# Kernel optimization log

Hardware: AMD Instinct MI355X
Metric: run time of the kernel (lower is better)

## Reference

```python
import jax, jax.numpy as jnp
from jax import lax
import numpy as np

EMBED = 1024
HIDDEN = 1024
VOCAB = 32000
T = 64


def setup_inputs() -> dict:
    key = jax.random.key(0)
    ks = jax.random.split(key, 8)
    s = 0.02  # weight init scale
    return {
        "captions": jax.random.randint(ks[0], (T,), 0, VOCAB, dtype=jnp.int32),
        "features": jax.random.normal(ks[1], (EMBED,), dtype=jnp.float32),
        "embed_table": jax.random.normal(ks[2], (VOCAB, EMBED), dtype=jnp.float32) * s,
        "W_ih": jax.random.normal(ks[3], (4 * HIDDEN, EMBED), dtype=jnp.float32) * s,
        "W_hh": jax.random.normal(ks[4], (4 * HIDDEN, HIDDEN), dtype=jnp.float32) * s,
        "b_ih": jnp.zeros((4 * HIDDEN,), dtype=jnp.float32),
        "b_hh": jnp.zeros((4 * HIDDEN,), dtype=jnp.float32),
        "fc_W": jax.random.normal(ks[5], (VOCAB, HIDDEN), dtype=jnp.float32) * s,
        "fc_b": jnp.zeros((VOCAB,), dtype=jnp.float32),
    }


def reference(captions, features, embed_table, W_ih, W_hh, b_ih, b_hh, fc_W, fc_b):
    # Embedding lookup for all caption tokens: [T, E]
    emb = embed_table[captions]
    # Input at t=0 is the visual feature; at t>0 it is embed(captions[t-1]).
    xs = jnp.concatenate([features[None, :], emb[:-1]], axis=0)  # [T, E]
    H = W_hh.shape[1]
    bias = b_ih + b_hh  # fuse the two LSTMCell biases

    def step(carry, x):
        h, c = carry  # [H], [H]  (batch = 1, kept 1-D)
        gates = x @ W_ih.T + h @ W_hh.T + bias  # [4H]
        i, f, g, o = jnp.split(gates, 4)  # PyTorch gate order: i, f, g, o
        i = jax.nn.sigmoid(i)
        f = jax.nn.sigmoid(f)
        g = jnp.tanh(g)
        o = jax.nn.sigmoid(o)
        c = f * c + i * g
        h = o * jnp.tanh(c)
        return (h, c), h

    h0 = jnp.zeros((H,), dtype=features.dtype)
    (_, _), hs = lax.scan(step, (h0, h0), xs)  # hs: [T, H]
    # Per-step Linear, expressed as one batched GEMM over all timesteps.
    logits = hs @ fc_W.T + fc_b  # [T, V]
    return logits[None, :, :]  # [1, T, V] to match outputs[:, t, :]
```

## Files before the change

kernel.cpp:

```cpp
#include <hip/hip_runtime.h>
#include <math.h>

#define EMBED  1024
#define HIDDEN 1024
#define VOCAB  32000
#define TSTEPS 64
#define NBLK   256

__global__ __launch_bounds__(256, 1) void decoder_fused(
    const int*   __restrict__ caps,
    const float* __restrict__ feat,
    const float* __restrict__ table,
    const float* __restrict__ Wih,
    const float* __restrict__ Whh,
    const float* __restrict__ bih,
    const float* __restrict__ bhh,
    const float* __restrict__ fcW,
    const float* __restrict__ fcb,
    unsigned long long* hs_pk,
    float* __restrict__ out)
{
    __shared__ __align__(16) char arena[52224];
    __shared__ float xg_s[TSTEPS][16];
    __shared__ float h_s[2][HIDDEN];
    __shared__ int   caps_s[TSTEPS];

    int tid = threadIdx.x;
    int b   = blockIdx.x;

    int lane = tid & 63;
    int wv   = tid >> 6;
    int g    = lane >> 4;
    int c16  = lane & 15;
    int hj   = 4 * b + wv;
    const float4* wrow = (const float4*)(Whh + ((size_t)g * HIDDEN + hj) * HIDDEN);
    float4 wreg[16];
#pragma unroll
    for (int k = 0; k < 16; ++k) wreg[k] = wrow[c16 + 16 * k];

    if (tid < TSTEPS) caps_s[tid] = caps[tid];

    float (*xs_s)[132] = (float (*)[132])arena;
    float (*w16)[132]  = (float (*)[132])(arena + 33792);
    int jl = tid & 15;
    int tg = tid >> 4;
    float acc4[4] = {0.f, 0.f, 0.f, 0.f};
    __syncthreads();

    for (int c = 0; c < 8; ++c) {
        __syncthreads();
        for (int idx = tid; idx < 64 * 32; idx += 256) {
            int r = idx >> 5, f4 = idx & 31;
            const float* src = (r == 0)
                ? (feat + c * 128)
                : (table + (size_t)caps_s[r - 1] * EMBED + c * 128);
            *((float4*)&xs_s[r][f4 * 4]) = ((const float4*)src)[f4];
        }
        for (int idx = tid; idx < 16 * 32; idx += 256) {
            int r = idx >> 5, f4 = idx & 31;
            int jr = (r >> 2) * HIDDEN + 4 * b + (r & 3);
            *((float4*)&w16[r][f4 * 4]) =
                ((const float4*)(Wih + (size_t)jr * EMBED + c * 128))[f4];
        }
        __syncthreads();
        for (int f4 = 0; f4 < 32; ++f4) {
            float4 w = *((const float4*)&w16[jl][f4 * 4]);
#pragma unroll
            for (int k = 0; k < 4; ++k) {
                const float* xr = &xs_s[tg * 4 + k][f4 * 4];
                acc4[k] += w.x * xr[0] + w.y * xr[1] + w.z * xr[2] + w.w * xr[3];
            }
        }
    }
    {
        int jrow = (jl >> 2) * HIDDEN + 4 * b + (jl & 3);
        float bias = bih[jrow] + bhh[jrow];
#pragma unroll
        for (int k = 0; k < 4; ++k) xg_s[tg * 4 + k][jl] = acc4[k] + bias;
    }
    __syncthreads();

    float cstate = 0.f;
    for (int t = 0; t < TSTEPS; ++t) {
        float* dst = h_s[t & 1];
        if (t == 0) {
            for (int i = tid; i < HIDDEN; i += 256) dst[i] = 0.f;
        } else {
            const unsigned long long* hsrc = hs_pk + (size_t)(t - 1) * HIDDEN;
            unsigned want = (unsigned)t;
            unsigned long long x0 = 0, x1 = 0, x2 = 0, x3 = 0;
            int need = 0xF;
            do {
                if (need & 1) {
                    x0 = __hip_atomic_load(hsrc + tid, __ATOMIC_RELAXED,
                                           __HIP_MEMORY_SCOPE_AGENT);
                    if ((unsigned)(x0 >> 32) == want) need &= ~1;
                }
                if (need & 2) {
                    x1 = __hip_atomic_load(hsrc + tid + 256, __ATOMIC_RELAXED,
                                           __HIP_MEMORY_SCOPE_AGENT);
                    if ((unsigned)(x1 >> 32) == want) need &= ~2;
                }
                if (need & 4) {
                    x2 = __hip_atomic_load(hsrc + tid + 512, __ATOMIC_RELAXED,
                                           __HIP_MEMORY_SCOPE_AGENT);
                    if ((unsigned)(x2 >> 32) == want) need &= ~4;
                }
                if (need & 8) {
                    x3 = __hip_atomic_load(hsrc + tid + 768, __ATOMIC_RELAXED,
                                           __HIP_MEMORY_SCOPE_AGENT);
                    if ((unsigned)(x3 >> 32) == want) need &= ~8;
                }
                if (need) __builtin_amdgcn_s_sleep(1);
            } while (need);
            dst[tid]       = __uint_as_float((unsigned)x0);
            dst[tid + 256] = __uint_as_float((unsigned)x1);
            dst[tid + 512] = __uint_as_float((unsigned)x2);
            dst[tid + 768] = __uint_as_float((unsigned)x3);
        }
        __syncthreads();

        float4 a = {0.f, 0.f, 0.f, 0.f};
#pragma unroll
        for (int k = 0; k < 16; ++k) {
            float4 w = wreg[k];
            const float* hv = &dst[(c16 + 16 * k) * 4];
            a.x += w.x * hv[0];
            a.y += w.y * hv[1];
            a.z += w.z * hv[2];
            a.w += w.w * hv[3];
        }
        float sum = (a.x + a.y) + (a.z + a.w);
        sum += __shfl_xor(sum, 1);
        sum += __shfl_xor(sum, 2);
        sum += __shfl_xor(sum, 4);
        sum += __shfl_xor(sum, 8);
        float s0 = __shfl(sum, 0);
        float s1 = __shfl(sum, 16);
        float s2 = __shfl(sum, 32);
        float s3 = __shfl(sum, 48);

        if (lane == 0) {
            float gi = s0 + xg_s[t][wv];
            float gf = s1 + xg_s[t][4 + wv];
            float gg = s2 + xg_s[t][8 + wv];
            float go = s3 + xg_s[t][12 + wv];
            float i_ = 1.f / (1.f + expf(-gi));
            float f_ = 1.f / (1.f + expf(-gf));
            float g_ = tanhf(gg);
            float o_ = 1.f / (1.f + expf(-go));
            cstate = f_ * cstate + i_ * g_;
            float hv = o_ * tanhf(cstate);
            unsigned long long pk =
                ((unsigned long long)(unsigned)(t + 1) << 32) |
                (unsigned long long)__float_as_uint(hv);
            __hip_atomic_store(hs_pk + (size_t)t * HIDDEN + hj, pk,
                               __ATOMIC_RELAXED, __HIP_MEMORY_SCOPE_AGENT);
        }
    }
    __syncthreads();

    if (b >= 250) return;
    float (*hs_s)[68]  = (float (*)[68])arena;
    float (*w_s3)[68]  = (float (*)[68])(arena + 17408);
    int tv = tid & 15;
    int tq = tid >> 4;
    int v0 = b * 128;
    float acc[4][8];
#pragma unroll
    for (int i = 0; i < 4; ++i)
#pragma unroll
        for (int j = 0; j < 8; ++j) acc[i][j] = 0.f;

    for (int kc = 0; kc < 16; ++kc) {
        __syncthreads();
        for (int idx = tid; idx < 64 * 64; idx += 256) {
            int t = idx >> 6, j = idx & 63;
            unsigned want = (unsigned)(t + 1);
            unsigned long long x;
            for (;;) {
                x = __hip_atomic_load(hs_pk + (size_t)t * HIDDEN + kc * 64 + j,
                                      __ATOMIC_RELAXED, __HIP_MEMORY_SCOPE_AGENT);
                if ((unsigned)(x >> 32) == want) break;
                __builtin_amdgcn_s_sleep(1);
            }
            hs_s[t][j] = __uint_as_float((unsigned)x);
        }
        for (int idx = tid; idx < 128 * 16; idx += 256) {
            int r = idx >> 4, f4 = idx & 15;
            *((float4*)&w_s3[r][f4 * 4]) =
                ((const float4*)(fcW + (size_t)(v0 + r) * HIDDEN + kc * 64))[f4];
        }
        __syncthreads();
        for (int q = 0; q < 16; ++q) {
            float4 hv4[4];
#pragma unroll
            for (int i = 0; i < 4; ++i)
                hv4[i] = *((const float4*)&hs_s[tq * 4 + i][q * 4]);
#pragma unroll
            for (int j = 0; j < 8; ++j) {
                float4 w4 = *((const float4*)&w_s3[tv + 16 * j][q * 4]);
#pragma unroll
                for (int i = 0; i < 4; ++i) {
                    acc[i][j] += w4.x * hv4[i].x + w4.y * hv4[i].y +
                                 w4.z * hv4[i].z + w4.w * hv4[i].w;
                }
            }
        }
    }
    float bj[8];
#pragma unroll
    for (int j = 0; j < 8; ++j) bj[j] = fcb[v0 + tv + 16 * j];
#pragma unroll
    for (int i = 0; i < 4; ++i)
#pragma unroll
        for (int j = 0; j < 8; ++j)
            out[(size_t)(tq * 4 + i) * VOCAB + v0 + tv + 16 * j] = acc[i][j] + bj[j];
}

extern "C" void kernel_launch(void* const* d_in, const int* in_sizes, int n_in,
                              void* d_out, int out_size, void* d_ws, size_t ws_size,
                              hipStream_t stream) {
    const int*   caps  = (const int*)  d_in[0];
    const float* feat  = (const float*)d_in[1];
    const float* table = (const float*)d_in[2];
    const float* Wih   = (const float*)d_in[3];
    const float* Whh   = (const float*)d_in[4];
    const float* bih   = (const float*)d_in[5];
    const float* bhh   = (const float*)d_in[6];
    const float* fcW   = (const float*)d_in[7];
    const float* fcb   = (const float*)d_in[8];
    float* out = (float*)d_out;

    unsigned long long* hs_pk = (unsigned long long*)d_ws;

    decoder_fused<<<NBLK, 256, 0, stream>>>(caps, feat, table, Wih, Whh,
                                            bih, bhh, fcW, fcb, hs_pk, out);
}
```

Measured before the change: 701.0 us.

## Interleave output projection GEMM into LSTM recurrence in 8-step groups

```diff
diff --git a/kernel.cpp b/kernel.cpp
--- a/kernel.cpp
+++ b/kernel.cpp
@@ -6,6 +6,8 @@
 #define VOCAB  32000
 #define TSTEPS 64
 #define NBLK   256
+#define HSTR   1028
+#define WSTR   68
 
 __global__ __launch_bounds__(256, 1) void decoder_fused(
     const int*   __restrict__ caps,
@@ -20,9 +22,8 @@
     unsigned long long* hs_pk,
     float* __restrict__ out)
 {
-    __shared__ __align__(16) char arena[52224];
+    __shared__ __align__(16) char arena[67712];
     __shared__ float xg_s[TSTEPS][16];
-    __shared__ float h_s[2][HIDDEN];
     __shared__ int   caps_s[TSTEPS];
 
     int tid = threadIdx.x;
@@ -40,49 +41,90 @@
 
     if (tid < TSTEPS) caps_s[tid] = caps[tid];
 
-    float (*xs_s)[132] = (float (*)[132])arena;
-    float (*w16)[132]  = (float (*)[132])(arena + 33792);
-    int jl = tid & 15;
-    int tg = tid >> 4;
-    float acc4[4] = {0.f, 0.f, 0.f, 0.f};
-    __syncthreads();
-
-    for (int c = 0; c < 8; ++c) {
-        __syncthreads();
-        for (int idx = tid; idx < 64 * 32; idx += 256) {
-            int r = idx >> 5, f4 = idx & 31;
-            const float* src = (r == 0)
-                ? (feat + c * 128)
-                : (table + (size_t)caps_s[r - 1] * EMBED + c * 128);
-            *((float4*)&xs_s[r][f4 * 4]) = ((const float4*)src)[f4];
-        }
-        for (int idx = tid; idx < 16 * 32; idx += 256) {
-            int r = idx >> 5, f4 = idx & 31;
-            int jr = (r >> 2) * HIDDEN + 4 * b + (r & 3);
-            *((float4*)&w16[r][f4 * 4]) =
-                ((const float4*)(Wih + (size_t)jr * EMBED + c * 128))[f4];
-        }
-        __syncthreads();
-        for (int f4 = 0; f4 < 32; ++f4) {
-            float4 w = *((const float4*)&w16[jl][f4 * 4]);
-#pragma unroll
-            for (int k = 0; k < 4; ++k) {
-                const float* xr = &xs_s[tg * 4 + k][f4 * 4];
-                acc4[k] += w.x * xr[0] + w.y * xr[1] + w.z * xr[2] + w.w * xr[3];
-            }
-        }
-    }
     {
+        float (*xs_s)[132] = (float (*)[132])arena;
+        float (*w16)[132]  = (float (*)[132])(arena + 33792);
+        int jl = tid & 15;
+        int tg = tid >> 4;
+        float acc4[4] = {0.f, 0.f, 0.f, 0.f};
+        __syncthreads();
+
+        for (int c = 0; c < 8; ++c) {
+            __syncthreads();
+            for (int idx = tid; idx < 64 * 32; idx += 256) {
+                int r = idx >> 5, f4 = idx & 31;
+                const float* src = (r == 0)
+                    ? (feat + c * 128)
+                    : (table + (size_t)caps_s[r - 1] * EMBED + c * 128);
+                *((float4*)&xs_s[r][f4 * 4]) = ((const float4*)src)[f4];
+            }
+            for (int idx = tid; idx < 16 * 32; idx += 256) {
+                int r = idx >> 5, f4 = idx & 31;
+                int jr = (r >> 2) * HIDDEN + 4 * b + (r & 3);
+                *((float4*)&w16[r][f4 * 4]) =
+                    ((const float4*)(Wih + (size_t)jr * EMBED + c * 128))[f4];
+            }
+            __syncthreads();
+            for (int f4 = 0; f4 < 32; ++f4) {
+                float4 w = *((const float4*)&w16[jl][f4 * 4]);
+#pragma unroll
+                for (int k = 0; k < 4; ++k) {
+                    float4 x4 = *((const float4*)&xs_s[tg * 4 + k][f4 * 4]);
+                    acc4[k] += w.x * x4.x + w.y * x4.y + w.z * x4.z + w.w * x4.w;
+                }
+            }
+        }
         int jrow = (jl >> 2) * HIDDEN + 4 * b + (jl & 3);
         float bias = bih[jrow] + bhh[jrow];
 #pragma unroll
         for (int k = 0; k < 4; ++k) xg_s[tg * 4 + k][jl] = acc4[k] + bias;
+        __syncthreads();
     }
-    __syncthreads();
+
+    float (*hist)[HSTR] = (float (*)[HSTR])arena;
+    float (*w3)[WSTR]   = (float (*)[WSTR])(arena + 32896);
+
+    int tt0 = (tid & 3) * 2;
+    int vv  = tid >> 2;
+    int v0  = b * 128;
+    float fb0 = 0.f, fb1 = 0.f;
+    if (b < 250) { fb0 = fcb[v0 + vv]; fb1 = fcb[v0 + vv + 64]; }
+
+    auto do_group = [&](int tg0) {
+        float a00 = 0.f, a01 = 0.f, a10 = 0.f, a11 = 0.f;
+        for (int kc = 0; kc < 16; ++kc) {
+            __syncthreads();
+#pragma unroll
+            for (int i = 0; i < 8; ++i) {
+                int idx = tid + i * 256;
+                int r = idx >> 4, f4 = idx & 15;
+                *((float4*)&w3[r][f4 * 4]) =
+                    ((const float4*)(fcW + (size_t)(v0 + r) * HIDDEN + kc * 64))[f4];
+            }
+            __syncthreads();
+#pragma unroll
+            for (int q4 = 0; q4 < 16; ++q4) {
+                float4 ha = *((const float4*)&hist[tt0    ][kc * 64 + q4 * 4]);
+                float4 hb = *((const float4*)&hist[tt0 + 1][kc * 64 + q4 * 4]);
+                float4 wa = *((const float4*)&w3[vv     ][q4 * 4]);
+                float4 wb = *((const float4*)&w3[vv + 64][q4 * 4]);
+                a00 += wa.x * ha.x + wa.y * ha.y + wa.z * ha.z + wa.w * ha.w;
+                a01 += wb.x * ha.x + wb.y * ha.y + wb.z * ha.z + wb.w * ha.w;
+                a10 += wa.x * hb.x + wa.y * hb.y + wa.z * hb.z + wa.w * hb.w;
+                a11 += wb.x * hb.x + wb.y * hb.y + wb.z * hb.z + wb.w * hb.w;
+            }
+        }
+        int tr = tg0 + tt0;
+        out[(size_t)tr * VOCAB + v0 + vv]            = a00 + fb0;
+        out[(size_t)tr * VOCAB + v0 + vv + 64]       = a01 + fb1;
+        out[(size_t)(tr + 1) * VOCAB + v0 + vv]      = a10 + fb0;
+        out[(size_t)(tr + 1) * VOCAB + v0 + vv + 64] = a11 + fb1;
+        __syncthreads();
+    };
 
     float cstate = 0.f;
     for (int t = 0; t < TSTEPS; ++t) {
-        float* dst = h_s[t & 1];
+        float* dst = hist[(t - 1) & 7];
         if (t == 0) {
             for (int i = tid; i < HIDDEN; i += 256) dst[i] = 0.f;
         } else {
@@ -119,6 +161,8 @@
             dst[tid + 768] = __uint_as_float((unsigned)x3);
         }
         __syncthreads();
+
+        if ((t & 7) == 0 && t > 0 && b < 250) do_group(t - 8);
 
         float4 a = {0.f, 0.f, 0.f, 0.f};
 #pragma unroll
@@ -158,64 +202,42 @@
                                __ATOMIC_RELAXED, __HIP_MEMORY_SCOPE_AGENT);
         }
     }
-    __syncthreads();
-
-    if (b >= 250) return;
-    float (*hs_s)[68]  = (float (*)[68])arena;
-    float (*w_s3)[68]  = (float (*)[68])(arena + 17408);
-    int tv = tid & 15;
-    int tq = tid >> 4;
-    int v0 = b * 128;
-    float acc[4][8];
-#pragma unroll
-    for (int i = 0; i < 4; ++i)
-#pragma unroll
-        for (int j = 0; j < 8; ++j) acc[i][j] = 0.f;
-
-    for (int kc = 0; kc < 16; ++kc) {
-        __syncthreads();
-        for (int idx = tid; idx < 64 * 64; idx += 256) {
-            int t = idx >> 6, j = idx & 63;
-            unsigned want = (unsigned)(t + 1);
-            unsigned long long x;
-            for (;;) {
-                x = __hip_atomic_load(hs_pk + (size_t)t * HIDDEN + kc * 64 + j,
-                                      __ATOMIC_RELAXED, __HIP_MEMORY_SCOPE_AGENT);
-                if ((unsigned)(x >> 32) == want) break;
-                __builtin_amdgcn_s_sleep(1);
-            }
-            hs_s[t][j] = __uint_as_float((unsigned)x);
-        }
-        for (int idx = tid; idx < 128 * 16; idx += 256) {
-            int r = idx >> 4, f4 = idx & 15;
-            *((float4*)&w_s3[r][f4 * 4]) =
-                ((const float4*)(fcW + (size_t)(v0 + r) * HIDDEN + kc * 64))[f4];
-        }
-        __syncthreads();
-        for (int q = 0; q < 16; ++q) {
-            float4 hv4[4];
-#pragma unroll
-            for (int i = 0; i < 4; ++i)
-                hv4[i] = *((const float4*)&hs_s[tq * 4 + i][q * 4]);
-#pragma unroll
-            for (int j = 0; j < 8; ++j) {
-                float4 w4 = *((const float4*)&w_s3[tv + 16 * j][q * 4]);
-#pragma unroll
-                for (int i = 0; i < 4; ++i) {
-                    acc[i][j] += w4.x * hv4[i].x + w4.y * hv4[i].y +
-                                 w4.z * hv4[i].z + w4.w * hv4[i].w;
-                }
-            }
-        }
+
+    {
+        const unsigned long long* hsrc = hs_pk + (size_t)63 * HIDDEN;
+        float* dst = hist[7];
+        unsigned long long x0 = 0, x1 = 0, x2 = 0, x3 = 0;
+        int need = 0xF;
+        do {
+            if (need & 1) {
+                x0 = __hip_atomic_load(hsrc + tid, __ATOMIC_RELAXED,
+                                       __HIP_MEMORY_SCOPE_AGENT);
+                if ((unsigned)(x0 >> 32) == 64u) need &= ~1;
+            }
+            if (need & 2) {
+                x1 = __hip_atomic_load(hsrc + tid + 256, __ATOMIC_RELAXED,
+                                       __HIP_MEMORY_SCOPE_AGENT);
+                if ((unsigned)(x1 >> 32) == 64u) need &= ~2;
+            }
+            if (need & 4) {
+                x2 = __hip_atomic_load(hsrc + tid + 512, __ATOMIC_RELAXED,
+                                       __HIP_MEMORY_SCOPE_AGENT);
+                if ((unsigned)(x2 >> 32) == 64u) need &= ~4;
+            }
+            if (need & 8) {
+                x3 = __hip_atomic_load(hsrc + tid + 768, __ATOMIC_RELAXED,
+                                       __HIP_MEMORY_SCOPE_AGENT);
+                if ((unsigned)(x3 >> 32) == 64u) need &= ~8;
+            }
+            if (need) __builtin_amdgcn_s_sleep(1);
+        } while (need);
+        dst[tid]       = __uint_as_float((unsigned)x0);
+        dst[tid + 256] = __uint_as_float((unsigned)x1);
+        dst[tid + 512] = __uint_as_float((unsigned)x2);
+        dst[tid + 768] = __uint_as_float((unsigned)x3);
+        __syncthreads();
     }
-    float bj[8];
-#pragma unroll
-    for (int j = 0; j < 8; ++j) bj[j] = fcb[v0 + tv + 16 * j];
-#pragma unroll
-    for (int i = 0; i < 4; ++i)
-#pragma unroll
-        for (int j = 0; j < 8; ++j)
-            out[(size_t)(tq * 4 + i) * VOCAB + v0 + tv + 16 * j] = acc[i][j] + bj[j];
+    if (b < 250) do_group(56);
 }
 
 extern "C" void kernel_launch(void* const* d_in, const int* in_sizes, int n_in,
```

Result: slower. 984.5 us (+40.4%).

## Use 1024 threads per block across all phases of the fused LSTM decoder kernel

Applied to the files above, without the earlier changes.

```diff
diff --git a/kernel.cpp b/kernel.cpp
--- a/kernel.cpp
+++ b/kernel.cpp
@@ -7,7 +7,7 @@
 #define TSTEPS 64
 #define NBLK   256
 
-__global__ __launch_bounds__(256, 1) void decoder_fused(
+__global__ __launch_bounds__(1024, 1) void decoder_fused(
     const int*   __restrict__ caps,
     const float* __restrict__ feat,
     const float* __restrict__ table,
@@ -25,197 +25,193 @@
     __shared__ float h_s[2][HIDDEN];
     __shared__ int   caps_s[TSTEPS];
 
-    int tid = threadIdx.x;
-    int b   = blockIdx.x;
-
+    int tid  = threadIdx.x;
+    int b    = blockIdx.x;
     int lane = tid & 63;
-    int wv   = tid >> 6;
-    int g    = lane >> 4;
-    int c16  = lane & 15;
-    int hj   = 4 * b + wv;
-    const float4* wrow = (const float4*)(Whh + ((size_t)g * HIDDEN + hj) * HIDDEN);
+
+    int wv  = tid >> 6;
+    int g   = lane >> 4;
+    int c16 = lane & 15;
+    int hj  = 4 * b + wv;
     float4 wreg[16];
-#pragma unroll
-    for (int k = 0; k < 16; ++k) wreg[k] = wrow[c16 + 16 * k];
-
+    if (tid < 256) {
+        const float4* wrow =
+            (const float4*)(Whh + ((size_t)g * HIDDEN + hj) * HIDDEN);
+#pragma unroll
+        for (int k = 0; k < 16; ++k) wreg[k] = wrow[c16 + 16 * k];
+    }
     if (tid < TSTEPS) caps_s[tid] = caps[tid];
 
-    float (*xs_s)[132] = (float (*)[132])arena;
-    float (*w16)[132]  = (float (*)[132])(arena + 33792);
-    int jl = tid & 15;
-    int tg = tid >> 4;
-    float acc4[4] = {0.f, 0.f, 0.f, 0.f};
-    __syncthreads();
-
-    for (int c = 0; c < 8; ++c) {
-        __syncthreads();
-        for (int idx = tid; idx < 64 * 32; idx += 256) {
-            int r = idx >> 5, f4 = idx & 31;
-            const float* src = (r == 0)
-                ? (feat + c * 128)
-                : (table + (size_t)caps_s[r - 1] * EMBED + c * 128);
-            *((float4*)&xs_s[r][f4 * 4]) = ((const float4*)src)[f4];
-        }
-        for (int idx = tid; idx < 16 * 32; idx += 256) {
-            int r = idx >> 5, f4 = idx & 31;
-            int jr = (r >> 2) * HIDDEN + 4 * b + (r & 3);
-            *((float4*)&w16[r][f4 * 4]) =
-                ((const float4*)(Wih + (size_t)jr * EMBED + c * 128))[f4];
-        }
-        __syncthreads();
-        for (int f4 = 0; f4 < 32; ++f4) {
-            float4 w = *((const float4*)&w16[jl][f4 * 4]);
-#pragma unroll
-            for (int k = 0; k < 4; ++k) {
-                const float* xr = &xs_s[tg * 4 + k][f4 * 4];
-                acc4[k] += w.x * xr[0] + w.y * xr[1] + w.z * xr[2] + w.w * xr[3];
-            }
-        }
-    }
     {
+        float (*xs_s)[132] = (float (*)[132])arena;
+        float (*w16)[132]  = (float (*)[132])(arena + 33792);
+        int jl = tid & 15;
+        int tg = tid >> 4;
+        float acc1 = 0.f;
+        __syncthreads();
+
+        for (int c = 0; c < 8; ++c) {
+            __syncthreads();
+#pragma unroll
+            for (int s = 0; s < 2; ++s) {
+                int idx = tid + s * 1024;
+                int r = idx >> 5, f4 = idx & 31;
+                const float* src = (r == 0)
+                    ? (feat + c * 128)
+                    : (table + (size_t)caps_s[r - 1] * EMBED + c * 128);
+                *((float4*)&xs_s[r][f4 * 4]) = ((const float4*)src)[f4];
+            }
+            if (tid < 512) {
+                int r = tid >> 5, f4 = tid & 31;
+                int jr = (r >> 2) * HIDDEN + 4 * b + (r & 3);
+                *((float4*)&w16[r][f4 * 4]) =
+                    ((const float4*)(Wih + (size_t)jr * EMBED + c * 128))[f4];
+            }
+            __syncthreads();
+            for (int f4 = 0; f4 < 32; ++f4) {
+                float4 w = *((const float4*)&w16[jl][f4 * 4]);
+                float4 x = *((const float4*)&xs_s[tg][f4 * 4]);
+                acc1 += w.x * x.x + w.y * x.y + w.z * x.z + w.w * x.w;
+            }
+        }
         int jrow = (jl >> 2) * HIDDEN + 4 * b + (jl & 3);
-        float bias = bih[jrow] + bhh[jrow];
-#pragma unroll
-        for (int k = 0; k < 4; ++k) xg_s[tg * 4 + k][jl] = acc4[k] + bias;
-    }
-    __syncthreads();
+        xg_s[tg][jl] = acc1 + bih[jrow] + bhh[jrow];
+        __syncthreads();
+    }
 
     float cstate = 0.f;
     for (int t = 0; t < TSTEPS; ++t) {
         float* dst = h_s[t & 1];
         if (t == 0) {
-            for (int i = tid; i < HIDDEN; i += 256) dst[i] = 0.f;
+            dst[tid] = 0.f;
         } else {
-            const unsigned long long* hsrc = hs_pk + (size_t)(t - 1) * HIDDEN;
+            const unsigned long long* src =
+                hs_pk + (size_t)(t - 1) * HIDDEN + tid;
             unsigned want = (unsigned)t;
-            unsigned long long x0 = 0, x1 = 0, x2 = 0, x3 = 0;
-            int need = 0xF;
-            do {
-                if (need & 1) {
-                    x0 = __hip_atomic_load(hsrc + tid, __ATOMIC_RELAXED,
-                                           __HIP_MEMORY_SCOPE_AGENT);
-                    if ((unsigned)(x0 >> 32) == want) need &= ~1;
-                }
-                if (need & 2) {
-                    x1 = __hip_atomic_load(hsrc + tid + 256, __ATOMIC_RELAXED,
-                                           __HIP_MEMORY_SCOPE_AGENT);
-                    if ((unsigned)(x1 >> 32) == want) need &= ~2;
-                }
-                if (need & 4) {
-                    x2 = __hip_atomic_load(hsrc + tid + 512, __ATOMIC_RELAXED,
-                                           __HIP_MEMORY_SCOPE_AGENT);
-                    if ((unsigned)(x2 >> 32) == want) need &= ~4;
-                }
-                if (need & 8) {
-                    x3 = __hip_atomic_load(hsrc + tid + 768, __ATOMIC_RELAXED,
-                                           __HIP_MEMORY_SCOPE_AGENT);
-                    if ((unsigned)(x3 >> 32) == want) need &= ~8;
-                }
-                if (need) __builtin_amdgcn_s_sleep(1);
-            } while (need);
-            dst[tid]       = __uint_as_float((unsigned)x0);
-            dst[tid + 256] = __uint_as_float((unsigned)x1);
-            dst[tid + 512] = __uint_as_float((unsigned)x2);
-            dst[tid + 768] = __uint_as_float((unsigned)x3);
-        }
-        __syncthreads();
-
-        float4 a = {0.f, 0.f, 0.f, 0.f};
-#pragma unroll
-        for (int k = 0; k < 16; ++k) {
-            float4 w = wreg[k];
-            const float* hv = &dst[(c16 + 16 * k) * 4];
-            a.x += w.x * hv[0];
-            a.y += w.y * hv[1];
-            a.z += w.z * hv[2];
-            a.w += w.w * hv[3];
-        }
-        float sum = (a.x + a.y) + (a.z + a.w);
-        sum += __shfl_xor(sum, 1);
-        sum += __shfl_xor(sum, 2);
-        sum += __shfl_xor(sum, 4);
-        sum += __shfl_xor(sum, 8);
-        float s0 = __shfl(sum, 0);
-        float s1 = __shfl(sum, 16);
-        float s2 = __shfl(sum, 32);
-        float s3 = __shfl(sum, 48);
-
-        if (lane == 0) {
-            float gi = s0 + xg_s[t][wv];
-            float gf = s1 + xg_s[t][4 + wv];
-            float gg = s2 + xg_s[t][8 + wv];
-            float go = s3 + xg_s[t][12 + wv];
-            float i_ = 1.f / (1.f + expf(-gi));
-            float f_ = 1.f / (1.f + expf(-gf));
-            float g_ = tanhf(gg);
-            float o_ = 1.f / (1.f + expf(-go));
-            cstate = f_ * cstate + i_ * g_;
-            float hv = o_ * tanhf(cstate);
-            unsigned long long pk =
-                ((unsigned long long)(unsigned)(t + 1) << 32) |
-                (unsigned long long)__float_as_uint(hv);
-            __hip_atomic_store(hs_pk + (size_t)t * HIDDEN + hj, pk,
-                               __ATOMIC_RELAXED, __HIP_MEMORY_SCOPE_AGENT);
+            unsigned long long x;
+            for (;;) {
+                x = __hip_atomic_load(src, __ATOMIC_RELAXED,
+                                      __HIP_MEMORY_SCOPE_AGENT);
+                if ((unsigned)(x >> 32) == want) break;
+                __builtin_amdgcn_s_sleep(1);
+            }
+            dst[tid] = __uint_as_float((unsigned)x);
+        }
+        __syncthreads();
+
+        if (tid < 256) {
+            float4 a = {0.f, 0.f, 0.f, 0.f};
+#pragma unroll
+            for (int k = 0; k < 16; ++k) {
+                float4 w = wreg[k];
+                const float* hv = &dst[(c16 + 16 * k) * 4];
+                a.x += w.x * hv[0];
+                a.y += w.y * hv[1];
+                a.z += w.z * hv[2];
+                a.w += w.w * hv[3];
+            }
+            float sum = (a.x + a.y) + (a.z + a.w);
+            sum += __shfl_xor(sum, 1);
+            sum += __shfl_xor(sum, 2);
+            sum += __shfl_xor(sum, 4);
+            sum += __shfl_xor(sum, 8);
+            float s0 = __shfl(sum, 0);
+            float s1 = __shfl(sum, 16);
+            float s2 = __shfl(sum, 32);
+            float s3 = __shfl(sum, 48);
+
+            if (lane == 0) {
+                float gi = s0 + xg_s[t][wv];
+                float gf = s1 + xg_s[t][4 + wv];
+                float gg = s2 + xg_s[t][8 + wv];
+                float go = s3 + xg_s[t][12 + wv];
+                float i_ = 1.f / (1.f + expf(-gi));
+                float f_ = 1.f / (1.f + expf(-gf));
+                float g_ = tanhf(gg);
+                float o_ = 1.f / (1.f + expf(-go));
+                cstate = f_ * cstate + i_ * g_;
+                float hv = o_ * tanhf(cstate);
+                unsigned long long pk =
+                    ((unsigned long long)(unsigned)(t + 1) << 32) |
+                    (unsigned long long)__float_as_uint(hv);
+                __hip_atomic_store(hs_pk + (size_t)t * HIDDEN + hj, pk,
+                                   __ATOMIC_RELAXED, __HIP_MEMORY_SCOPE_AGENT);
+            }
         }
     }
     __syncthreads();
 
     if (b >= 250) return;
-    float (*hs_s)[68]  = (float (*)[68])arena;
-    float (*w_s3)[68]  = (float (*)[68])(arena + 17408);
+    float (*hs_s)[68] = (float (*)[68])arena;
+    float (*w3)[68]   = (float (*)[68])(arena + 17408);
     int tv = tid & 15;
     int tq = tid >> 4;
     int v0 = b * 128;
-    float acc[4][8];
-#pragma unroll
-    for (int i = 0; i < 4; ++i)
-#pragma unroll
-        for (int j = 0; j < 8; ++j) acc[i][j] = 0.f;
+    float acc[8];
+#pragma unroll
+    for (int j = 0; j < 8; ++j) acc[j] = 0.f;
+
+    int jcol  = tid & 63;
+    int trow0 = tid >> 6;
 
     for (int kc = 0; kc < 16; ++kc) {
-        __syncthreads();
-        for (int idx = tid; idx < 64 * 64; idx += 256) {
-            int t = idx >> 6, j = idx & 63;
-            unsigned want = (unsigned)(t + 1);
-            unsigned long long x;
+        unsigned long long v4[4];
+        {
+            const unsigned long long* src = hs_pk + kc * 64 + jcol;
             for (;;) {
-                x = __hip_atomic_load(hs_pk + (size_t)t * HIDDEN + kc * 64 + j,
-                                      __ATOMIC_RELAXED, __HIP_MEMORY_SCOPE_AGENT);
-                if ((unsigned)(x >> 32) == want) break;
-                __builtin_amdgcn_s_sleep(1);
-            }
-            hs_s[t][j] = __uint_as_float((unsigned)x);
-        }
-        for (int idx = tid; idx < 128 * 16; idx += 256) {
+#pragma unroll
+                for (int i = 0; i < 4; ++i)
+                    v4[i] = __hip_atomic_load(
+                        src + (size_t)(trow0 + 16 * i) * HIDDEN,
+                        __ATOMIC_RELAXED, __HIP_MEMORY_SCOPE_AGENT);
+                bool ok = true;
+#pragma unroll
+                for (int i = 0; i < 4; ++i)
+                    ok &= ((unsigned)(v4[i] >> 32) ==
+                           (unsigned)(trow0 + 16 * i + 1));
+                if (ok) break;
+                __builtin_amdgcn_s_sleep(8);
+            }
+        }
+        __syncthreads();
+#pragma unroll
+        for (int i = 0; i < 4; ++i)
+            hs_s[trow0 + 16 * i][jcol] = __uint_as_float((unsigned)v4[i]);
+#pragma unroll
+        for (int s = 0; s < 2; ++s) {
+            int idx = tid + s * 1024;
             int r = idx >> 4, f4 = idx & 15;
-            *((float4*)&w_s3[r][f4 * 4]) =
+            *((float4*)&w3[r][f4 * 4]) =
                 ((const float4*)(fcW + (size_t)(v0 + r) * HIDDEN + kc * 64))[f4];
         }
         __syncthreads();
         for (int q = 0; q < 16; ++q) {
-            float4 hv4[4];
-#pragma unroll
-            for (int i = 0; i < 4; ++i)
-                hv4[i] = *((const float4*)&hs_s[tq * 4 + i][q * 4]);
+            float4 hv = *((const float4*)&hs_s[tq][q * 4]);
 #pragma unroll
             for (int j = 0; j < 8; ++j) {
-                float4 w4 = *((const float4*)&w_s3[tv + 16 * j][q * 4]);
-#pragma unroll
-                for (int i = 0; i < 4; ++i) {
-                    acc[i][j] += w4.x * hv4[i].x + w4.y * hv4[i].y +
-                                 w4.z * hv4[i].z + w4.w * hv4[i].w;
-                }
-            }
-        }
-    }
-    float bj[8];
-#pragma unroll
-    for (int j = 0; j < 8; ++j) bj[j] = fcb[v0 + tv + 16 * j];
-#pragma unroll
-    for (int i = 0; i < 4; ++i)
-#pragma unroll
-        for (int j = 0; j < 8; ++j)
-            out[(size_t)(tq * 4 + i) * VOCAB + v0 + tv + 16 * j] = acc[i][j] + bj[j];
+                float4 w4 = *((const float4*)&w3[tv + 16 * j][q * 4]);
+                acc[j] += w4.x * hv.x + w4.y * hv.y +
+                          w4.z * hv.z + w4.w * hv.w;
+            }
+        }
+    }
+
+    float (*ot)[132] = (float (*)[132])(arena + 17408);
+    __syncthreads();
+#pragma unroll
+    for (int j = 0; j < 8; ++j)
+        ot[tq][tv + 16 * j] = acc[j] + fcb[v0 + tv + 16 * j];
+    __syncthreads();
+    {
+        int col4 = tid & 31;
+        int row  = tid >> 5;
+#pragma unroll
+        for (int rep = 0; rep < 2; ++rep) {
+            int r = row + 32 * rep;
+            float4 o = *((const float4*)&ot[r][col4 * 4]);
+            *((float4*)&out[(size_t)r * VOCAB + v0 + col4 * 4]) = o;
+        }
+    }
 }
 
 extern "C" void kernel_launch(void* const* d_in, const int* in_sizes, int n_in,
@@ -234,6 +230,6 @@
 
     unsigned long long* hs_pk = (unsigned long long*)d_ws;
 
-    decoder_fused<<<NBLK, 256, 0, stream>>>(caps, feat, table, Wih, Whh,
-                                            bih, bhh, fcW, fcb, hs_pk, out);
+    decoder_fused<<<NBLK, 1024, 0, stream>>>(caps, feat, table, Wih, Whh,
+                                             bih, bhh, fcW, fcb, hs_pk, out);
 }
```

Result: faster. 653.2 us (-6.8%).
